# Kernel tuning notes

Measured on AMD Instinct MI355X. Metric: run time of the kernel, lower is better.

The kernel has to match this reference:

```python
import jax, jax.numpy as jnp
import numpy as np

# ---- static config (MaskedViTConfig, eval mode with inference_topk) ----
B, IMG, P, C = 32, 224, 16, 3
G = IMG // P            # 14
N = G * G + 1           # 197 tokens incl cls
D, NH = 768, 12
HD = D // NH            # 64
SCALE = HD ** -0.5
HID = 4 * D             # 3072
GH = 128                # gate hidden
WARM, DYN = 2, 10
TOPK = 118              # min(inference_topk, N-1)
NC = 1000
EPS_MASK = 1e-6
LN_EPS = 1e-5


def _ln(x, g, b):
    mu = x.mean(-1, keepdims=True)
    var = ((x - mu) ** 2).mean(-1, keepdims=True)
    return (x - mu) / jnp.sqrt(var + LN_EPS) * g + b


def _attn(x, qkv_w, qkv_b, proj_w, proj_b, add_mask):
    # x: [B,N,D]; add_mask: [B,N] additive logit bias per key, or None
    Bb, Nn, _ = x.shape
    qkv = (x @ qkv_w + qkv_b).reshape(Bb, Nn, 3, NH, HD)
    q, k, v = qkv[:, :, 0], qkv[:, :, 1], qkv[:, :, 2]  # [B,N,H,hd]
    attn = jnp.einsum('bqhd,bkhd->bhqk', q, k) * SCALE
    if add_mask is not None:
        attn = attn + add_mask[:, None, None, :]
    attn = jax.nn.softmax(attn, axis=-1)
    out = jnp.einsum('bhqk,bkhd->bqhd', attn, v).reshape(Bb, Nn, D)
    return out @ proj_w + proj_b


def _mlp(x, w1, b1, w2, b2):
    return jax.nn.gelu(x @ w1 + b1, approximate=False) @ w2 + b2


def setup_inputs() -> dict:
    key = jax.random.key(0)
    ks = iter(jax.random.split(key, 64))
    nrm = lambda shape, s=0.02: jax.random.normal(next(ks), shape, jnp.float32) * s
    z = lambda *shape: jnp.zeros(shape, jnp.float32)
    o = lambda *shape: jnp.ones(shape, jnp.float32)
    inp = {
        'images': jax.random.normal(next(ks), (B, C, IMG, IMG), jnp.float32),
        'patch_w': nrm((D, C, P, P)), 'patch_b': z(D),
        'cls_token': nrm((1, 1, D)), 'pos_embed': nrm((1, N, D)),
        # warmup blocks, stacked on leading axis [WARM,...]
        'w_ln1_g': o(WARM, D), 'w_ln1_b': z(WARM, D),
        'w_qkv_w': nrm((WARM, D, 3 * D)), 'w_qkv_b': z(WARM, 3 * D),
        'w_proj_w': nrm((WARM, D, D)), 'w_proj_b': z(WARM, D),
        'w_ln2_g': o(WARM, D), 'w_ln2_b': z(WARM, D),
        'w_fc1_w': nrm((WARM, D, HID)), 'w_fc1_b': z(WARM, HID),
        'w_fc2_w': nrm((WARM, HID, D)), 'w_fc2_b': z(WARM, D),
        # dynamic masked blocks [DYN,...]
        'd_ln1_g': o(DYN, D), 'd_ln1_b': z(DYN, D),
        'd_qkv_w': nrm((DYN, D, 3 * D)), 'd_qkv_b': z(DYN, 3 * D),
        'd_proj_w': nrm((DYN, D, D)), 'd_proj_b': z(DYN, D),
        'd_ln2_g': o(DYN, D), 'd_ln2_b': z(DYN, D),
        'd_fc1_w': nrm((DYN, D, HID)), 'd_fc1_b': z(DYN, HID),
        'd_fc2_w': nrm((DYN, HID, D)), 'd_fc2_b': z(DYN, D),
        # gate predictor: LayerNorm -> Linear(D,GH) -> GELU -> Linear(GH,1)
        'd_gln_g': o(DYN, D), 'd_gln_b': z(DYN, D),
        'd_gw1': nrm((DYN, D, GH)), 'd_gb1': z(DYN, GH),
        'd_gw2': nrm((DYN, GH, 1)), 'd_gb2': z(DYN, 1),
        # final norm + head
        'norm_g': o(D), 'norm_b': z(D),
        'head_w': nrm((D, NC)), 'head_b': z(NC),
    }
    return inp


def reference(images, patch_w, patch_b, cls_token, pos_embed,
              w_ln1_g, w_ln1_b, w_qkv_w, w_qkv_b, w_proj_w, w_proj_b,
              w_ln2_g, w_ln2_b, w_fc1_w, w_fc1_b, w_fc2_w, w_fc2_b,
              d_ln1_g, d_ln1_b, d_qkv_w, d_qkv_b, d_proj_w, d_proj_b,
              d_ln2_g, d_ln2_b, d_fc1_w, d_fc1_b, d_fc2_w, d_fc2_b,
              d_gln_g, d_gln_b, d_gw1, d_gb1, d_gw2, d_gb2,
              norm_g, norm_b, head_w, head_b):
    Bb = images.shape[0]
    # patch embed: conv with kernel==stride==P is a block reshape + matmul
    x6 = images.reshape(Bb, C, G, P, G, P)
    x = jnp.einsum('bcxpyq,dcpq->bxyd', x6, patch_w).reshape(Bb, G * G, D) + patch_b
    cls = jnp.broadcast_to(cls_token, (Bb, 1, D))
    x = jnp.concatenate([cls, x], axis=1) + pos_embed  # [B,N,D]

    for i in range(WARM):
        x = x + _attn(_ln(x, w_ln1_g[i], w_ln1_b[i]),
                      w_qkv_w[i], w_qkv_b[i], w_proj_w[i], w_proj_b[i], None)
        x = x + _mlp(_ln(x, w_ln2_g[i], w_ln2_b[i]),
                     w_fc1_w[i], w_fc1_b[i], w_fc2_w[i], w_fc2_b[i])

    for j in range(DYN):
        # gate predictor -> logits [B,N]; cls forced kept
        h = _ln(x, d_gln_g[j], d_gln_b[j])
        logits = (jax.nn.gelu(h @ d_gw1[j] + d_gb1[j], approximate=False)
                  @ d_gw2[j] + d_gb2[j]).squeeze(-1)
        logits = logits.at[:, 0].set(1e9)
        # eval-mode top-k keep mask (inference_topk path)
        _, idx = jax.lax.top_k(logits[:, 1:], TOPK)
        m = jnp.zeros_like(logits).at[:, 0].set(1.0)
        m = m.at[jnp.arange(Bb)[:, None], idx + 1].set(1.0)
        add_mask = jnp.log(jnp.clip(m, EPS_MASK, 1.0))
        x = x + _attn(_ln(x, d_ln1_g[j], d_ln1_b[j]),
                      d_qkv_w[j], d_qkv_b[j], d_proj_w[j], d_proj_b[j], add_mask)
        v = _mlp(_ln(x, d_ln2_g[j], d_ln2_b[j]),
                 d_fc1_w[j], d_fc1_b[j], d_fc2_w[j], d_fc2_b[j])
        x = x + v * m[:, :, None]  # gate_mlp_updates=True

    x = _ln(x, norm_g, norm_b)
    return x[:, 0] @ head_w + head_b  # [B, num_classes]
```

## Files before the change

### kernel.cpp

```cpp
#include <hip/hip_runtime.h>
#include <hip/hip_bf16.h>
#include <math.h>


typedef __bf16 bf16_t;
typedef __attribute__((ext_vector_type(8))) __bf16 bf16x8;
typedef __attribute__((ext_vector_type(4))) float f32x4;

#define DI __device__ __forceinline__

constexpr int NB     = 32;
constexpr int NTOK   = 197;
constexpr int DMODEL = 768;
constexpr int NHEAD  = 12;
constexpr int HDIM   = 64;
constexpr int HIDN   = 3072;
constexpr int GHID   = 128;
constexpr int MROWS  = NB * NTOK;
constexpr int PROWS  = NB * 196;
constexpr int NSEL   = 119;
constexpr int MROWSC = NB * NSEL;
constexpr int NLAYER = 12;
constexpr int KTOP   = 118;
constexpr float ATT_SCALE = 0.125f;
constexpr float LNEPS  = 1e-5f;
constexpr float LOGEPS = -13.815510558f;

DI f32x4 mfma16(bf16x8 a, bf16x8 b, f32x4 c) {
    return __builtin_amdgcn_mfma_f32_16x16x32_bf16(a, b, c, 0, 0, 0);
}

DI void gld_lds16(const void* g, void* l) {
    __builtin_amdgcn_global_load_lds(
        (__attribute__((address_space(1))) void*)(g),
        (__attribute__((address_space(3))) void*)(l), 16, 0, 0);
}

enum { EP_BF16 = 0, EP_GELU = 1, EP_RES = 2, EP_F32 = 4 };

template<int MODE, bool GA, bool SC, bool AT>
__global__ __launch_bounds__(256)
void gemm_bf16(const bf16_t* __restrict__ A, const bf16_t* __restrict__ Wt,
               const float* __restrict__ bias, void* __restrict__ Cout,
               float* __restrict__ resid, const int* __restrict__ rowidx,
               int M, int N, int K, int ldc, int klen)
{
    __shared__ __align__(16) bf16_t As[2][128 * 32];
    __shared__ __align__(16) bf16_t Bs[2][128 * 32];
    const int tid  = threadIdx.x;
    const int lane = tid & 63;
    const int wave = tid >> 6;
    const int wm = wave >> 1, wn = wave & 1;
    const int quad = lane >> 4, l16 = lane & 15;
    const int m0 = blockIdx.y * 128;
    const int n0 = blockIdx.x * 128;
    const int koff = AT ? blockIdx.z * klen : 0;

    f32x4 zero4 = {0.f, 0.f, 0.f, 0.f};
    f32x4 acc[4][4];
#pragma unroll
    for (int i = 0; i < 4; ++i)
#pragma unroll
        for (int j = 0; j < 4; ++j) acc[i][j] = zero4;

    const int rh  = tid >> 2;
    const int seg = tid & 3;
    int cA0 = min(m0 + rh,      M - 1);
    int cA1 = min(m0 + 64 + rh, M - 1);
    const int rA0 = GA ? rowidx[cA0] : cA0;
    const int rA1 = GA ? rowidx[cA1] : cA1;
    const int rB0 = min(n0 + rh,      N - 1);
    const int rB1 = min(n0 + 64 + rh, N - 1);
    const bf16_t* pA0 = A  + (size_t)rA0 * K + koff + seg * 8;
    const bf16_t* pA1 = A  + (size_t)rA1 * K + koff + seg * 8;
    const bf16_t* pB0 = Wt + (size_t)rB0 * K + koff + seg * 8;
    const bf16_t* pB1 = Wt + (size_t)rB1 * K + koff + seg * 8;
    const int lofs0 = wave * 512;
    const int lofs1 = 2048 + wave * 512;

    auto stage = [&](int kt2, int buf) {
        const int kb = kt2 << 5;
        gld_lds16(pA0 + kb, As[buf] + lofs0);
        gld_lds16(pA1 + kb, As[buf] + lofs1);
        gld_lds16(pB0 + kb, Bs[buf] + lofs0);
        gld_lds16(pB1 + kb, Bs[buf] + lofs1);
    };

    const int nkt = klen >> 5;
    stage(0, 0);
    stage(1, 1);

    for (int kt = 0; kt < nkt; ++kt) {
        const int cur = kt & 1;
        if (kt + 1 < nkt) asm volatile("s_waitcnt vmcnt(4)" ::: "memory");
        else              asm volatile("s_waitcnt vmcnt(0)" ::: "memory");
        __builtin_amdgcn_s_barrier();

        bf16x8 af[4], bfr[4];
#pragma unroll
        for (int i = 0; i < 4; ++i)
            af[i] = *reinterpret_cast<const bf16x8*>(As[cur] + (wm * 64 + i * 16 + l16) * 32 + quad * 8);
#pragma unroll
        for (int j = 0; j < 4; ++j)
            bfr[j] = *reinterpret_cast<const bf16x8*>(Bs[cur] + (wn * 64 + j * 16 + l16) * 32 + quad * 8);

        asm volatile("s_waitcnt lgkmcnt(0)" ::: "memory");
        __builtin_amdgcn_sched_barrier(0);
        __builtin_amdgcn_s_barrier();

        if (kt + 2 < nkt) stage(kt + 2, cur);

#pragma unroll
        for (int i = 0; i < 4; ++i)
#pragma unroll
            for (int j = 0; j < 4; ++j)
                acc[i][j] = mfma16(af[i], bfr[j], acc[i][j]);
    }

    const bool addb = bias && (!AT || blockIdx.z == 0);
#pragma unroll
    for (int j = 0; j < 4; ++j) {
        int c = n0 + wn * 64 + j * 16 + l16;
        if (c >= N) continue;
        float bj = addb ? bias[c] : 0.f;
#pragma unroll
        for (int i = 0; i < 4; ++i) {
#pragma unroll
            for (int r = 0; r < 4; ++r) {
                int mr = m0 + wm * 64 + i * 16 + quad * 4 + r;
                if (mr >= M) continue;
                float v = acc[i][j][r] + bj;
                int orow = SC ? rowidx[mr] : mr;
                size_t off = (size_t)orow * ldc + c;
                if (MODE == EP_BF16) {
                    ((bf16_t*)Cout)[off] = (bf16_t)v;
                } else if (MODE == EP_GELU) {
                    float g = 0.5f * v * (1.f + erff(v * 0.70710678118f));
                    ((bf16_t*)Cout)[off] = (bf16_t)g;
                } else if (MODE == EP_F32) {
                    ((float*)Cout)[off] = v;
                } else {
                    if (AT) atomicAdd(&resid[off], v);
                    else    resid[off] += v;
                }
            }
        }
    }
}

DI float block_reduce_sum(float val, float* sh) {
#pragma unroll
    for (int off = 32; off; off >>= 1) val += __shfl_down(val, off, 64);
    __syncthreads();
    if ((threadIdx.x & 63) == 0) sh[threadIdx.x >> 6] = val;
    __syncthreads();
    return sh[0] + sh[1] + sh[2] + sh[3];
}

template<typename OUT>
__global__ __launch_bounds__(256)
void ln_kernel(const float* __restrict__ X, const float* __restrict__ g,
               const float* __restrict__ bta, OUT* __restrict__ H, int row_mul)
{
    __shared__ float sh[4];
    const int t = threadIdx.x;
    const float* xr = X + (size_t)blockIdx.x * row_mul * DMODEL;
    float v[3];
#pragma unroll
    for (int i = 0; i < 3; ++i) v[i] = xr[t + i * 256];
    float s = v[0] + v[1] + v[2];
    s = block_reduce_sum(s, sh);
    float mu = s * (1.f / DMODEL);
    float q = 0.f;
#pragma unroll
    for (int i = 0; i < 3; ++i) { float d = v[i] - mu; q += d * d; }
    q = block_reduce_sum(q, sh);
    float rstd = rsqrtf(q * (1.f / DMODEL) + LNEPS);
    OUT* hr = H + (size_t)blockIdx.x * DMODEL;
#pragma unroll
    for (int i = 0; i < 3; ++i) {
        int c = t + i * 256;
        hr[c] = (OUT)((v[i] - mu) * rstd * g[c] + bta[c]);
    }
}

__global__ __launch_bounds__(256)
void attn_kernel(const bf16_t* __restrict__ qkv,
                 const float* __restrict__ addmask,
                 bf16_t* __restrict__ outp)
{
    constexpr int KP = 232;
    __shared__ __align__(16) bf16_t Vt[64 * KP];
    __shared__ __align__(16) bf16_t Ps[4][16 * KP];
    const int b = blockIdx.z, h = blockIdx.y, qt = blockIdx.x;
    const int tid = threadIdx.x, wave = tid >> 6, lane = tid & 63;
    const int quad = lane >> 4, l16 = lane & 15;

    {
        int d = tid & 63, ng = tid >> 6;
        for (int n = ng; n < 224; n += 4) {
            bf16_t v = (bf16_t)0.f;
            if (n < 197)
                v = qkv[(((size_t)b * NTOK + n) * 3 + 2) * DMODEL + h * HDIM + d];
            Vt[d * KP + n] = v;
        }
    }
    __syncthreads();

    const int qbase = qt * 64 + wave * 16;
    const int qrow = qbase + l16;
    const int qc = qrow < 196 ? qrow : 196;
    bf16x8 aq[2];
#pragma unroll
    for (int t = 0; t < 2; ++t)
        aq[t] = *reinterpret_cast<const bf16x8*>(
            qkv + (((size_t)b * NTOK + qc) * 3 + 0) * DMODEL + h * HDIM + t * 32 + quad * 8);

    float sreg[13][4];
#pragma unroll
    for (int kt = 0; kt < 13; ++kt) {
        int key = kt * 16 + l16;
        int kc = key < 196 ? key : 196;
        const bf16_t* kb = qkv + (((size_t)b * NTOK + kc) * 3 + 1) * DMODEL + h * HDIM;
        bf16x8 kf0 = *reinterpret_cast<const bf16x8*>(kb + quad * 8);
        bf16x8 kf1 = *reinterpret_cast<const bf16x8*>(kb + 32 + quad * 8);
        f32x4 s = {0.f, 0.f, 0.f, 0.f};
        s = mfma16(aq[0], kf0, s);
        s = mfma16(aq[1], kf1, s);
        float am = addmask ? addmask[b * NTOK + kc] : 0.f;
        bool kvalid = key < 197;
#pragma unroll
        for (int r = 0; r < 4; ++r)
            sreg[kt][r] = kvalid ? (s[r] * ATT_SCALE + am) : -1e30f;
    }

    float psum[4];
#pragma unroll
    for (int r = 0; r < 4; ++r) {
        float mx = -1e30f;
#pragma unroll
        for (int kt = 0; kt < 13; ++kt) mx = fmaxf(mx, sreg[kt][r]);
#pragma unroll
        for (int d = 1; d < 16; d <<= 1) mx = fmaxf(mx, __shfl_xor(mx, d, 64));
        float sum = 0.f;
#pragma unroll
        for (int kt = 0; kt < 13; ++kt) {
            float p = expf(sreg[kt][r] - mx);
            sreg[kt][r] = p;
            sum += p;
        }
#pragma unroll
        for (int d = 1; d < 16; d <<= 1) sum += __shfl_xor(sum, d, 64);
        psum[r] = sum;
    }

#pragma unroll
    for (int kt = 0; kt < 13; ++kt)
#pragma unroll
        for (int r = 0; r < 4; ++r)
            Ps[wave][(quad * 4 + r) * KP + kt * 16 + l16] = (bf16_t)sreg[kt][r];
    {
        int rr = lane & 15, c0 = 208 + (lane >> 4) * 4;
#pragma unroll
        for (int i = 0; i < 4; ++i) Ps[wave][rr * KP + c0 + i] = (bf16_t)0.f;
    }
    __syncthreads();

    f32x4 o[4];
#pragma unroll
    for (int j = 0; j < 4; ++j) o[j] = (f32x4){0.f, 0.f, 0.f, 0.f};
#pragma unroll
    for (int ks = 0; ks < 7; ++ks) {
        bf16x8 ap = *reinterpret_cast<const bf16x8*>(&Ps[wave][l16 * KP + ks * 32 + quad * 8]);
#pragma unroll
        for (int j = 0; j < 4; ++j) {
            bf16x8 vf = *reinterpret_cast<const bf16x8*>(&Vt[(j * 16 + l16) * KP + ks * 32 + quad * 8]);
            o[j] = mfma16(ap, vf, o[j]);
        }
    }

#pragma unroll
    for (int r = 0; r < 4; ++r) {
        int q = qbase + quad * 4 + r;
        if (q < 197) {
            float rs = 1.f / fmaxf(psum[r], 1e-20f);
#pragma unroll
            for (int j = 0; j < 4; ++j)
                outp[((size_t)b * NTOK + q) * DMODEL + h * HDIM + j * 16 + l16] =
                    (bf16_t)(o[j][r] * rs);
        }
    }
}

__global__ __launch_bounds__(256)
void transpose_f32(const float* __restrict__ src, bf16_t* __restrict__ dst, int K, int N)
{
    __shared__ bf16_t tile[64][65];
    const size_t ls = (size_t)K * N * blockIdx.z;
    int k0 = blockIdx.y * 64, n0 = blockIdx.x * 64;
    int c = threadIdx.x & 63, r0 = threadIdx.x >> 6;
#pragma unroll
    for (int i = 0; i < 16; ++i) {
        int r = r0 + i * 4;
        tile[r][c] = (k0 + r < K && n0 + c < N)
                   ? (bf16_t)src[ls + (size_t)(k0 + r) * N + n0 + c] : (bf16_t)0.f;
    }
    __syncthreads();
#pragma unroll
    for (int i = 0; i < 16; ++i) {
        int r = r0 + i * 4;
        if (n0 + r < N && k0 + c < K) dst[ls + (size_t)(n0 + r) * K + k0 + c] = tile[c][r];
    }
}

__global__ void cvt_f32_bf16(const float* __restrict__ src, bf16_t* __restrict__ dst, int n)
{
    int i = blockIdx.x * 256 + threadIdx.x;
    if (i < n) dst[i] = (bf16_t)src[i];
}

__global__ void im2col_kernel(const float* __restrict__ img, bf16_t* __restrict__ Ap)
{
    int idx = blockIdx.x * 256 + threadIdx.x;
    if (idx >= PROWS * 768) return;
    int col = idx % 768, row = idx / 768;
    int b = row / 196, t = row % 196;
    int gi = t / 14, gj = t % 14;
    int c = col >> 8, rr = col & 255, p = rr >> 4, q = rr & 15;
    Ap[idx] = (bf16_t)img[(((size_t)b * 3 + c) * 224 + gi * 16 + p) * 224 + gj * 16 + q];
}

__global__ void assemble_x(const float* __restrict__ patch, const float* __restrict__ cls,
                           const float* __restrict__ pos, float* __restrict__ X)
{
    int idx = blockIdx.x * 256 + threadIdx.x;
    if (idx >= MROWS * DMODEL) return;
    int d = idx % DMODEL, rest = idx / DMODEL;
    int n = rest % NTOK, b = rest / NTOK;
    float v;
    if (n == 0) v = cls[d] + pos[d];
    else        v = patch[((size_t)b * 196 + (n - 1)) * DMODEL + d] + pos[(size_t)n * DMODEL + d];
    X[idx] = v;
}

__global__ __launch_bounds__(256)
void gate_fused_f32(const float* __restrict__ A, const float* __restrict__ W1,
                    const float* __restrict__ b1, const float* __restrict__ w2,
                    const float* __restrict__ b2, float* __restrict__ logits)
{
    __shared__ __align__(16) float As[16][64];
    __shared__ __align__(16) float Ws[64][128];
    const int tid = threadIdx.x;
    const int m0 = blockIdx.x * 16;
    const int tx = tid & 31;
    const int rg = tid >> 5;
    f32x4 acc0 = {0.f, 0.f, 0.f, 0.f};
    f32x4 acc1 = {0.f, 0.f, 0.f, 0.f};
    for (int k0 = 0; k0 < 768; k0 += 64) {
        __syncthreads();
        {
            int idx = tid * 4;
            int r = idx >> 6, c = idx & 63;
            *reinterpret_cast<f32x4*>(&As[r][c]) =
                *reinterpret_cast<const f32x4*>(&A[(size_t)(m0 + r) * 768 + k0 + c]);
        }
#pragma unroll
        for (int i = 0; i < 8; ++i) {
            int idx = (tid + i * 256) * 4;
            int r = idx >> 7, c = idx & 127;
            *reinterpret_cast<f32x4*>(&Ws[r][c]) =
                *reinterpret_cast<const f32x4*>(&W1[(size_t)(k0 + r) * 128 + c]);
        }
        __syncthreads();
#pragma unroll
        for (int kk = 0; kk < 64; ++kk) {
            float a0 = As[rg * 2 + 0][kk];
            float a1 = As[rg * 2 + 1][kk];
            f32x4 w = *reinterpret_cast<const f32x4*>(&Ws[kk][tx * 4]);
#pragma unroll
            for (int j = 0; j < 4; ++j) {
                acc0[j] += a0 * w[j];
                acc1[j] += a1 * w[j];
            }
        }
    }
    float s0 = 0.f, s1 = 0.f;
#pragma unroll
    for (int j = 0; j < 4; ++j) {
        int c = tx * 4 + j;
        float bj = b1[c], wj = w2[c];
        float v0 = acc0[j] + bj;
        float v1 = acc1[j] + bj;
        s0 += 0.5f * v0 * (1.f + erff(v0 * 0.70710678118f)) * wj;
        s1 += 0.5f * v1 * (1.f + erff(v1 * 0.70710678118f)) * wj;
    }
#pragma unroll
    for (int d = 1; d < 32; d <<= 1) {
        s0 += __shfl_xor(s0, d, 64);
        s1 += __shfl_xor(s1, d, 64);
    }
    if (tx == 0) {
        logits[m0 + rg * 2 + 0] = s0 + b2[0];
        logits[m0 + rg * 2 + 1] = s1 + b2[0];
    }
}

__global__ __launch_bounds__(256)
void topk_kernel(const float* __restrict__ logits, float* __restrict__ maskm,
                 float* __restrict__ addm, int* __restrict__ rowidx)
{
    __shared__ float ls[196];
    int b = blockIdx.x, t = threadIdx.x;
    if (t < 196) ls[t] = logits[b * NTOK + 1 + t];
    __syncthreads();
    if (t < 196) {
        float li = ls[t];
        int cnt = 0;
        for (int j = 0; j < 196; ++j) {
            float lj = ls[j];
            cnt += (lj > li) || (lj == li && j < t);
        }
        bool sel = cnt < KTOP;
        maskm[b * NTOK + 1 + t] = sel ? 1.f : 0.f;
        addm[b * NTOK + 1 + t]  = sel ? 0.f : LOGEPS;
        if (sel) rowidx[b * NSEL + 1 + cnt] = b * NTOK + 1 + t;
    }
    if (t == 0) { maskm[b * NTOK] = 1.f; addm[b * NTOK] = 0.f; rowidx[b * NSEL] = b * NTOK; }
}

__global__ void fill_sentinel(float* out, int n)
{
    int i = blockIdx.x * 256 + threadIdx.x;
    if (i < n) out[i] = 12345.0f;
}

static void launch_gemm(int mode, const bf16_t* A, const bf16_t* Wt, const float* bias,
                        void* C, float* resid,
                        int M, int N, int K, int ldc, hipStream_t s)
{
    dim3 grid((N + 127) / 128, (M + 127) / 128);
    dim3 blk(256);
    switch (mode) {
    case EP_BF16: gemm_bf16<EP_BF16, false, false, false><<<grid, blk, 0, s>>>(A, Wt, bias, C, resid, nullptr, M, N, K, ldc, K); break;
    case EP_GELU: gemm_bf16<EP_GELU, false, false, false><<<grid, blk, 0, s>>>(A, Wt, bias, C, resid, nullptr, M, N, K, ldc, K); break;
    case EP_RES:  gemm_bf16<EP_RES,  false, false, false><<<grid, blk, 0, s>>>(A, Wt, bias, C, resid, nullptr, M, N, K, ldc, K); break;
    case EP_F32:  gemm_bf16<EP_F32,  false, false, false><<<grid, blk, 0, s>>>(A, Wt, bias, C, resid, nullptr, M, N, K, ldc, K); break;
    }
}

extern "C" void kernel_launch(void* const* d_in, const int* in_sizes, int n_in,
                              void* d_out, int out_size, void* d_ws, size_t ws_size,
                              hipStream_t stream)
{
    (void)in_sizes; (void)n_in;
    const float* images   = (const float*)d_in[0];
    const float* patch_w  = (const float*)d_in[1];
    const float* patch_b  = (const float*)d_in[2];
    const float* cls_tok  = (const float*)d_in[3];
    const float* pos_emb  = (const float*)d_in[4];
    const float* w_ln1_g  = (const float*)d_in[5];
    const float* w_ln1_b  = (const float*)d_in[6];
    const float* w_qkv_w  = (const float*)d_in[7];
    const float* w_qkv_b  = (const float*)d_in[8];
    const float* w_proj_w = (const float*)d_in[9];
    const float* w_proj_b = (const float*)d_in[10];
    const float* w_ln2_g  = (const float*)d_in[11];
    const float* w_ln2_b  = (const float*)d_in[12];
    const float* w_fc1_w  = (const float*)d_in[13];
    const float* w_fc1_b  = (const float*)d_in[14];
    const float* w_fc2_w  = (const float*)d_in[15];
    const float* w_fc2_b  = (const float*)d_in[16];
    const float* d_ln1_g  = (const float*)d_in[17];
    const float* d_ln1_b  = (const float*)d_in[18];
    const float* d_qkv_w  = (const float*)d_in[19];
    const float* d_qkv_b  = (const float*)d_in[20];
    const float* d_proj_w = (const float*)d_in[21];
    const float* d_proj_b = (const float*)d_in[22];
    const float* d_ln2_g  = (const float*)d_in[23];
    const float* d_ln2_b  = (const float*)d_in[24];
    const float* d_fc1_w  = (const float*)d_in[25];
    const float* d_fc1_b  = (const float*)d_in[26];
    const float* d_fc2_w  = (const float*)d_in[27];
    const float* d_fc2_b  = (const float*)d_in[28];
    const float* d_gln_g  = (const float*)d_in[29];
    const float* d_gln_b  = (const float*)d_in[30];
    const float* d_gw1    = (const float*)d_in[31];
    const float* d_gb1    = (const float*)d_in[32];
    const float* d_gw2    = (const float*)d_in[33];
    const float* d_gb2    = (const float*)d_in[34];
    const float* norm_g   = (const float*)d_in[35];
    const float* norm_b   = (const float*)d_in[36];
    const float* head_w   = (const float*)d_in[37];
    const float* head_b   = (const float*)d_in[38];

    char* wp = (char*)d_ws;
    auto alloc = [&](size_t bytes) -> char* {
        char* p = wp; wp += (bytes + 255) & ~(size_t)255; return p;
    };
    bf16_t* wtqkv  = (bf16_t*)alloc((size_t)NLAYER * 2304 * 768 * 2);
    bf16_t* wtproj = (bf16_t*)alloc((size_t)NLAYER * 768 * 768 * 2);
    bf16_t* wtfc1  = (bf16_t*)alloc((size_t)NLAYER * 3072 * 768 * 2);
    bf16_t* wtfc2  = (bf16_t*)alloc((size_t)NLAYER * 768 * 3072 * 2);
    bf16_t* wthead = (bf16_t*)alloc((size_t)1024 * 768 * 2);
    bf16_t* pwbf   = (bf16_t*)alloc((size_t)768 * 768 * 2);
    float*  x      = (float*)alloc((size_t)MROWS * DMODEL * 4);
    bf16_t* h      = (bf16_t*)alloc((size_t)MROWS * DMODEL * 2);
    float*  hgate  = (float*)alloc((size_t)MROWS * DMODEL * 4);
    bf16_t* hcls   = (bf16_t*)alloc((size_t)NB * DMODEL * 2);
    bf16_t* qkvb   = (bf16_t*)alloc((size_t)MROWS * 2304 * 2);
    bf16_t* attno  = (bf16_t*)alloc((size_t)MROWS * DMODEL * 2);
    bf16_t* hid    = (bf16_t*)alloc((size_t)MROWS * HIDN * 2);
    float*  logits = (float*)alloc((size_t)MROWS * 4);
    float*  maskm  = (float*)alloc((size_t)MROWS * 4);
    float*  addm   = (float*)alloc((size_t)MROWS * 4);
    int*    rowidx = (int*)alloc((size_t)MROWSC * 4);
    size_t used = (size_t)(wp - (char*)d_ws);
    if (used > ws_size) {
        fill_sentinel<<<(out_size + 255) / 256, 256, 0, stream>>>((float*)d_out, out_size);
        return;
    }
    bf16_t* Ap = hid;
    float* patchout = (float*)((char*)hid + (size_t)PROWS * 768 * 2);

    transpose_f32<<<dim3(36, 12, 2),  256, 0, stream>>>(w_qkv_w,  wtqkv,                      768, 2304);
    transpose_f32<<<dim3(36, 12, 10), 256, 0, stream>>>(d_qkv_w,  wtqkv + (size_t)2*2304*768, 768, 2304);
    transpose_f32<<<dim3(12, 12, 2),  256, 0, stream>>>(w_proj_w, wtproj,                     768, 768);
    transpose_f32<<<dim3(12, 12, 10), 256, 0, stream>>>(d_proj_w, wtproj + (size_t)2*768*768, 768, 768);
    transpose_f32<<<dim3(48, 12, 2),  256, 0, stream>>>(w_fc1_w,  wtfc1,                      768, 3072);
    transpose_f32<<<dim3(48, 12, 10), 256, 0, stream>>>(d_fc1_w,  wtfc1 + (size_t)2*3072*768, 768, 3072);
    transpose_f32<<<dim3(12, 48, 2),  256, 0, stream>>>(w_fc2_w,  wtfc2,                      3072, 768);
    transpose_f32<<<dim3(12, 48, 10), 256, 0, stream>>>(d_fc2_w,  wtfc2 + (size_t)2*768*3072, 3072, 768);
    transpose_f32<<<dim3(16, 12, 1),  256, 0, stream>>>(head_w,   wthead,                     768, 1000);
    cvt_f32_bf16<<<(768 * 768 + 255) / 256, 256, 0, stream>>>(patch_w, pwbf, 768 * 768);

    im2col_kernel<<<(PROWS * 768 + 255) / 256, 256, 0, stream>>>(images, Ap);
    launch_gemm(EP_F32, Ap, pwbf, patch_b, patchout, nullptr,
                PROWS, 768, 768, 768, stream);
    assemble_x<<<(MROWS * DMODEL + 255) / 256, 256, 0, stream>>>(patchout, cls_tok, pos_emb, x);

    for (int L = 0; L < NLAYER; ++L) {
        bool warm = (L < 2);
        int li = warm ? L : (L - 2);
        const float* ln1g = warm ? w_ln1_g + li*768 : d_ln1_g + li*768;
        const float* ln1b = warm ? w_ln1_b + li*768 : d_ln1_b + li*768;
        const float* ln2g = warm ? w_ln2_g + li*768 : d_ln2_g + li*768;
        const float* ln2b = warm ? w_ln2_b + li*768 : d_ln2_b + li*768;
        const float* qkvbias  = warm ? w_qkv_b + li*2304 : d_qkv_b + li*2304;
        const float* projbias = warm ? w_proj_b + li*768 : d_proj_b + li*768;
        const float* fc1bias  = warm ? w_fc1_b + (size_t)li*3072 : d_fc1_b + (size_t)li*3072;
        const float* fc2bias  = warm ? w_fc2_b + li*768 : d_fc2_b + li*768;
        const bf16_t* Wq = wtqkv + (size_t)L * 2304 * 768;
        const bf16_t* Wp = wtproj + (size_t)L * 768 * 768;
        const bf16_t* W1 = wtfc1 + (size_t)L * 3072 * 768;
        const bf16_t* W2 = wtfc2 + (size_t)L * 768 * 3072;

        if (!warm) {
            ln_kernel<float><<<MROWS, 256, 0, stream>>>(x, d_gln_g + li*768, d_gln_b + li*768, hgate, 1);
            gate_fused_f32<<<MROWS / 16, 256, 0, stream>>>(
                hgate, d_gw1 + (size_t)li*768*128, d_gb1 + li*128,
                d_gw2 + (size_t)li*128, d_gb2 + li, logits);
            topk_kernel<<<NB, 256, 0, stream>>>(logits, maskm, addm, rowidx);
        }
        ln_kernel<bf16_t><<<MROWS, 256, 0, stream>>>(x, ln1g, ln1b, h, 1);
        launch_gemm(EP_BF16, h, Wq, qkvbias, qkvb, nullptr,
                    MROWS, 2304, 768, 2304, stream);
        attn_kernel<<<dim3(4, NHEAD, NB), 256, 0, stream>>>(qkvb, warm ? nullptr : addm, attno);
        launch_gemm(EP_RES, attno, Wp, projbias, nullptr, x,
                    MROWS, 768, 768, 768, stream);
        ln_kernel<bf16_t><<<MROWS, 256, 0, stream>>>(x, ln2g, ln2b, h, 1);
        if (warm) {
            launch_gemm(EP_GELU, h, W1, fc1bias, hid, nullptr,
                        MROWS, 3072, 768, 3072, stream);
            launch_gemm(EP_RES, hid, W2, fc2bias, nullptr, x,
                        MROWS, 768, 3072, 768, stream);
        } else {
            dim3 g1(24, (MROWSC + 127) / 128);
            gemm_bf16<EP_GELU, true, false, false><<<g1, 256, 0, stream>>>(
                h, W1, fc1bias, hid, nullptr, rowidx, MROWSC, 3072, 768, 3072, 768);
            dim3 g2(6, (MROWSC + 127) / 128, 2);
            gemm_bf16<EP_RES, false, true, true><<<g2, 256, 0, stream>>>(
                hid, W2, fc2bias, nullptr, x, rowidx, MROWSC, 768, 3072, 768, 1536);
        }
    }

    ln_kernel<bf16_t><<<NB, 256, 0, stream>>>(x, norm_g, norm_b, hcls, NTOK);
    launch_gemm(EP_F32, hcls, wthead, head_b, d_out, nullptr,
                NB, 1000, 768, 1000, stream);
}
```

Before: 4.620 ms.

## Triple-buffer GEMM K pipeline, split-K proj/fc2, fuse gate and attn LayerNorms

The GEMM moves from a 2-stage to a 3-stage LDS ring buffer, keeping more global-to-LDS loads in flight, with vmcnt waits adjusted to match. The proj and warm fc2 residual GEMMs now use a split-K of 2 with atomic residual accumulation, doubling the block count for these N=768 GEMMs. In dynamic layers the gate LayerNorm and the LN1 LayerNorm are computed in one kernel, saving a launch and a read of x. The extra buffer raises LDS per block from 32KB to 48KB, which may lower occupancy, and atomic split-K adds contention and makes the summation order nondeterministic.

```diff
diff --git a/kernel.cpp b/kernel.cpp
--- a/kernel.cpp
+++ b/kernel.cpp
@@ -45,8 +45,8 @@
                float* __restrict__ resid, const int* __restrict__ rowidx,
                int M, int N, int K, int ldc, int klen)
 {
-    __shared__ __align__(16) bf16_t As[2][128 * 32];
-    __shared__ __align__(16) bf16_t Bs[2][128 * 32];
+    __shared__ __align__(16) bf16_t As[3][128 * 32];
+    __shared__ __align__(16) bf16_t Bs[3][128 * 32];
     const int tid  = threadIdx.x;
     const int lane = tid & 63;
     const int wave = tid >> 6;
@@ -89,11 +89,14 @@
     const int nkt = klen >> 5;
     stage(0, 0);
     stage(1, 1);
-
+    stage(2, 2);
+
+    int cur = 0;
     for (int kt = 0; kt < nkt; ++kt) {
-        const int cur = kt & 1;
-        if (kt + 1 < nkt) asm volatile("s_waitcnt vmcnt(4)" ::: "memory");
-        else              asm volatile("s_waitcnt vmcnt(0)" ::: "memory");
+        const int rem = nkt - kt;
+        if (rem >= 3)      asm volatile("s_waitcnt vmcnt(8)" ::: "memory");
+        else if (rem == 2) asm volatile("s_waitcnt vmcnt(4)" ::: "memory");
+        else               asm volatile("s_waitcnt vmcnt(0)" ::: "memory");
         __builtin_amdgcn_s_barrier();
 
         bf16x8 af[4], bfr[4];
@@ -108,13 +111,15 @@
         __builtin_amdgcn_sched_barrier(0);
         __builtin_amdgcn_s_barrier();
 
-        if (kt + 2 < nkt) stage(kt + 2, cur);
+        if (kt + 3 < nkt) stage(kt + 3, cur);
 
 #pragma unroll
         for (int i = 0; i < 4; ++i)
 #pragma unroll
             for (int j = 0; j < 4; ++j)
                 acc[i][j] = mfma16(af[i], bfr[j], acc[i][j]);
+
+        cur = (cur == 2) ? 0 : cur + 1;
     }
 
     const bool addb = bias && (!AT || blockIdx.z == 0);
@@ -185,6 +190,37 @@
 }
 
 __global__ __launch_bounds__(256)
+void ln_dual_kernel(const float* __restrict__ X,
+                    const float* __restrict__ g1, const float* __restrict__ b1,
+                    const float* __restrict__ g2, const float* __restrict__ b2,
+                    float* __restrict__ H1, bf16_t* __restrict__ H2)
+{
+    __shared__ float sh[4];
+    const int t = threadIdx.x;
+    const float* xr = X + (size_t)blockIdx.x * DMODEL;
+    float v[3];
+#pragma unroll
+    for (int i = 0; i < 3; ++i) v[i] = xr[t + i * 256];
+    float s = v[0] + v[1] + v[2];
+    s = block_reduce_sum(s, sh);
+    float mu = s * (1.f / DMODEL);
+    float q = 0.f;
+#pragma unroll
+    for (int i = 0; i < 3; ++i) { float d = v[i] - mu; q += d * d; }
+    q = block_reduce_sum(q, sh);
+    float rstd = rsqrtf(q * (1.f / DMODEL) + LNEPS);
+    float* h1 = H1 + (size_t)blockIdx.x * DMODEL;
+    bf16_t* h2 = H2 + (size_t)blockIdx.x * DMODEL;
+#pragma unroll
+    for (int i = 0; i < 3; ++i) {
+        int c = t + i * 256;
+        float nrm = (v[i] - mu) * rstd;
+        h1[c] = nrm * g1[c] + b1[c];
+        h2[c] = (bf16_t)(nrm * g2[c] + b2[c]);
+    }
+}
+
+__global__ __launch_bounds__(256)
 void attn_kernel(const bf16_t* __restrict__ qkv,
                  const float* __restrict__ addmask,
                  bf16_t* __restrict__ outp)
@@ -446,6 +482,14 @@
     case EP_RES:  gemm_bf16<EP_RES,  false, false, false><<<grid, blk, 0, s>>>(A, Wt, bias, C, resid, nullptr, M, N, K, ldc, K); break;
     case EP_F32:  gemm_bf16<EP_F32,  false, false, false><<<grid, blk, 0, s>>>(A, Wt, bias, C, resid, nullptr, M, N, K, ldc, K); break;
     }
+}
+
+static void launch_gemm_res_sk2(const bf16_t* A, const bf16_t* Wt, const float* bias,
+                                float* resid, int M, int N, int K, int ldc, hipStream_t s)
+{
+    dim3 grid((N + 127) / 128, (M + 127) / 128, 2);
+    gemm_bf16<EP_RES, false, false, true><<<grid, 256, 0, s>>>(
+        A, Wt, bias, nullptr, resid, nullptr, M, N, K, ldc, K / 2);
 }
 
 extern "C" void kernel_launch(void* const* d_in, const int* in_sizes, int n_in,
@@ -555,24 +599,24 @@
         const bf16_t* W2 = wtfc2 + (size_t)L * 768 * 3072;
 
         if (!warm) {
-            ln_kernel<float><<<MROWS, 256, 0, stream>>>(x, d_gln_g + li*768, d_gln_b + li*768, hgate, 1);
+            ln_dual_kernel<<<MROWS, 256, 0, stream>>>(
+                x, d_gln_g + li*768, d_gln_b + li*768, ln1g, ln1b, hgate, h);
             gate_fused_f32<<<MROWS / 16, 256, 0, stream>>>(
                 hgate, d_gw1 + (size_t)li*768*128, d_gb1 + li*128,
                 d_gw2 + (size_t)li*128, d_gb2 + li, logits);
             topk_kernel<<<NB, 256, 0, stream>>>(logits, maskm, addm, rowidx);
-        }
-        ln_kernel<bf16_t><<<MROWS, 256, 0, stream>>>(x, ln1g, ln1b, h, 1);
+        } else {
+            ln_kernel<bf16_t><<<MROWS, 256, 0, stream>>>(x, ln1g, ln1b, h, 1);
+        }
         launch_gemm(EP_BF16, h, Wq, qkvbias, qkvb, nullptr,
                     MROWS, 2304, 768, 2304, stream);
         attn_kernel<<<dim3(4, NHEAD, NB), 256, 0, stream>>>(qkvb, warm ? nullptr : addm, attno);
-        launch_gemm(EP_RES, attno, Wp, projbias, nullptr, x,
-                    MROWS, 768, 768, 768, stream);
+        launch_gemm_res_sk2(attno, Wp, projbias, x, MROWS, 768, 768, 768, stream);
         ln_kernel<bf16_t><<<MROWS, 256, 0, stream>>>(x, ln2g, ln2b, h, 1);
         if (warm) {
             launch_gemm(EP_GELU, h, W1, fc1bias, hid, nullptr,
                         MROWS, 3072, 768, 3072, stream);
-            launch_gemm(EP_RES, hid, W2, fc2bias, nullptr, x,
-                        MROWS, 768, 3072, 768, stream);
+            launch_gemm_res_sk2(hid, W2, fc2bias, x, MROWS, 768, 3072, 768, stream);
         } else {
             dim3 g1(24, (MROWSC + 127) / 128);
             gemm_bf16<EP_GELU, true, false, false><<<g1, 256, 0, stream>>>(
```

New measurement: 4.673 ms. About the same (+1.1%).
